# Kernel optimization log

Measured on AMD Instinct MI355X. Metric: run time of the kernel, lower is better.

The kernel has to match this reference:

```python
import jax, jax.numpy as jnp
import numpy as np

DIM = 512
HEADS = 8
DIM_HEAD = 64
HIDDEN = HEADS * DIM_HEAD  # 512
B, H, W = 32, 64, 64


def setup_inputs() -> dict:
    key = jax.random.key(0)
    k1, k2, k3 = jax.random.split(key, 3)
    x = jax.random.normal(k1, (B, H, W, DIM), dtype=jnp.float32)
    w_qkv = jax.random.normal(k2, (DIM, 3 * HIDDEN), dtype=jnp.float32) * 0.02
    w_out = jax.random.normal(k3, (HIDDEN, DIM), dtype=jnp.float32) * 0.02
    b_out = jnp.zeros((DIM,), dtype=jnp.float32)
    return {"x": x, "w_qkv": w_qkv, "w_out": w_out, "b_out": b_out}


def reference(x, w_qkv, w_out, b_out):
    b, h, w, c = x.shape
    n = h * w
    scale = DIM_HEAD ** (-0.5)
    # 1x1 conv (no bias) == matmul over channels
    qkv = jnp.einsum('bhwc,cf->bhwf', x, w_qkv)  # (b, h, w, 3*hidden)
    q, k, v = jnp.split(qkv, 3, axis=-1)
    # 'b x y (h c) -> b (x y) h c'
    def to_heads(t):
        return t.reshape(b, n, HEADS, DIM_HEAD)
    q, k, v = map(to_heads, (q, k, v))
    q = q * scale
    # contraction over spatial axis d=(x*y): sim (b, dim_head_i, heads, dim_head_j)
    sim = jnp.einsum('bdhi,bdhj->bihj', q, k)
    sim = sim - jnp.max(sim, axis=-1, keepdims=True)
    attn = jax.nn.softmax(sim, axis=-1)
    out = jnp.einsum('bihj,bdhj->bdhi', attn, v)  # (b, n, heads, dim_head)
    out = out.reshape(b, h, w, HIDDEN)
    # output 1x1 conv with bias
    return jnp.einsum('bhwf,fc->bhwc', out, w_out) + b_out
```

## Files before the change

kernel.cpp:

```cpp
#include <hip/hip_runtime.h>
#include <hip/hip_bf16.h>
#include <stdint.h>

using bf16x8 = __attribute__((ext_vector_type(8))) __bf16;
using s16x8  = __attribute__((ext_vector_type(8))) short;
using f32x4  = __attribute__((ext_vector_type(4))) float;

__device__ __forceinline__ uint16_t f2bf(float f) {
    uint32_t u = __builtin_bit_cast(uint32_t, f);
    u += 0x7fffu + ((u >> 16) & 1u);
    return (uint16_t)(u >> 16);
}
__device__ __forceinline__ float bf2f(uint16_t h) {
    return __builtin_bit_cast(float, (uint32_t)h << 16);
}

__device__ __forceinline__ void async16(uint16_t* lds_dst, const uint16_t* g_src) {
    __builtin_amdgcn_global_load_lds(
        (const __attribute__((address_space(1))) void*)g_src,
        (__attribute__((address_space(3))) void*)lds_dst,
        16, 0, 0);
}

__global__ __launch_bounds__(256, 4)
void xtw_k(const float* __restrict__ x, const float* __restrict__ wqkv,
           const float* __restrict__ wout,
           uint16_t* __restrict__ xb, uint16_t* __restrict__ xT,
           uint16_t* __restrict__ wqTs, uint16_t* __restrict__ wkTcat,
           uint16_t* __restrict__ woutT, uint16_t* __restrict__ wv_rm)
{
    __shared__ uint16_t lt[64 * 68];
    const int tid = threadIdx.x;
    const int bi = blockIdx.x;
    if (bi >= 16384) {
        int sec = (bi - 16384) >> 10;
        int idx = ((bi - 16384) & 1023) * 256 + tid;
        int co = idx >> 9, r = idx & 511;
        if (sec == 0) {
            wqTs[co * 512 + r] = f2bf(wqkv[r * 1536 + co] * 0.125f);
        } else if (sec == 1) {
            uint16_t v = f2bf(wqkv[r * 1536 + 512 + co]);
            wkTcat[co * 1024 + r] = v;
            wkTcat[co * 1024 + 512 + r] = v;
        } else if (sec == 2) {
            woutT[co * 512 + r] = f2bf(wout[r * 512 + co]);
        } else {
            wv_rm[co * 512 + r] = f2bf(wqkv[co * 1536 + 1024 + r]);
        }
        return;
    }
    const int b = bi >> 9;
    const int rem = bi & 511;
    const int st = rem >> 3, ct = rem & 7;
    const int c4 = (tid & 15) * 4;
#pragma unroll
    for (int rep = 0; rep < 4; ++rep) {
        int r = (tid >> 4) + rep * 16;
        long gs = (long)(b * 4096 + st * 64 + r) * 512 + ct * 64 + c4;
        float4 v = *(const float4*)(x + gs);
        uint16_t t[4];
        t[0] = f2bf(v.x); t[1] = f2bf(v.y); t[2] = f2bf(v.z); t[3] = f2bf(v.w);
        *(ushort4*)(xb + gs) = *(const ushort4*)t;
#pragma unroll
        for (int q = 0; q < 4; ++q) lt[r * 68 + c4 + q] = t[q];
    }
    __syncthreads();
    const int s4 = (tid & 15) * 4;
#pragma unroll
    for (int rep = 0; rep < 4; ++rep) {
        int c = (tid >> 4) + rep * 16;
        uint16_t t[4];
#pragma unroll
        for (int q = 0; q < 4; ++q) t[q] = lt[(s4 + q) * 68 + c];
        *(ushort4*)(xT + (long)(b * 512 + ct * 64 + c) * 4096 + st * 64 + s4) =
            *(const ushort4*)t;
    }
}

template<bool OUTF32>
__global__ __launch_bounds__(512, 2)
void g8_k(const uint16_t* __restrict__ A, const uint16_t* __restrict__ Bt,
          void* __restrict__ Cp, const float* __restrict__ bias,
          int K, int lda, int ldb, int ldc, int mtiles, int ntiles,
          long abr, long bbe, long cbr)
{
    __shared__ uint16_t lds[65536];
    const int tid  = threadIdx.x;
    const int lane = tid & 63;
    const int wv   = tid >> 6;
    const int wr   = wv >> 2, wc = wv & 3;

    const int q8 = gridDim.x >> 3;
    const int l  = (blockIdx.x & 7) * q8 + (blockIdx.x >> 3);
    const int per   = mtiles * ntiles;
    const int batch = l / per;
    const int rem   = l - batch * per;
    const int mt    = rem / ntiles, nt = rem - mt * ntiles;

    const long arow0 = abr * batch + (long)mt * 256;
    const uint16_t* abase = A + arow0 * (long)lda;
    const uint16_t* btb   = Bt + bbe * batch + (long)nt * 256 * ldb;

    const int fr = lane & 15;
    const int cx0 = (((0 << 2) | (lane >> 4)) ^ (fr & 7)) * 8;
    const int cx1 = (((1 << 2) | (lane >> 4)) ^ (fr & 7)) * 8;
    const int baseA = wr * 8192 + fr * 64;
    const int baseB = (2 + (wc >> 1)) * 8192 + ((wc & 1) * 64 + fr) * 64;

    const int NT = K >> 6;

    auto stage = [&](int slot, const uint16_t* gb, int rstride, int k0) {
#pragma unroll
        for (int i = 0; i < 2; ++i) {
            int si = i * 512 + wv * 64 + lane;
            int rr = si >> 3, cc = (si & 7) ^ (rr & 7);
            async16(&lds[slot * 8192 + (i * 512 + wv * 64) * 8],
                    gb + (long)rr * rstride + k0 + cc * 8);
        }
    };

    f32x4 acc[8][4];
#pragma unroll
    for (int m = 0; m < 8; ++m)
#pragma unroll
        for (int n = 0; n < 4; ++n) acc[m][n] = (f32x4){0.f, 0.f, 0.f, 0.f};

    bf16x8 af[4], bfq[4];

    auto rdA = [&](int mb, int b4, int cx) {
#pragma unroll
        for (int mi = 0; mi < 4; ++mi)
            af[mi] = __builtin_bit_cast(bf16x8,
                *(const s16x8*)&lds[b4 * 8192 + baseA + (mb + mi) * 1024 + cx]);
    };
    auto rdB = [&](int b4, int cx) {
#pragma unroll
        for (int n = 0; n < 4; ++n)
            bfq[n] = __builtin_bit_cast(bf16x8,
                *(const s16x8*)&lds[b4 * 8192 + baseB + n * 1024 + cx]);
    };
    auto mm = [&](int mb) {
        asm volatile("s_waitcnt lgkmcnt(0)" ::: "memory");
        __builtin_amdgcn_sched_barrier(0);
        __builtin_amdgcn_s_setprio(1);
#pragma unroll
        for (int mi = 0; mi < 4; ++mi)
#pragma unroll
            for (int n = 0; n < 4; ++n)
                acc[mb + mi][n] = __builtin_amdgcn_mfma_f32_16x16x32_bf16(
                    af[mi], bfq[n], acc[mb + mi][n], 0, 0, 0);
        __builtin_amdgcn_s_setprio(0);
        __builtin_amdgcn_s_barrier();
    };

    stage(0, abase,              lda, 0);
    stage(1, abase + 128L * lda, lda, 0);
    stage(2, btb,                ldb, 0);
    stage(3, btb + 128L * ldb,   ldb, 0);
    stage(6, btb,                ldb, 64);
    stage(7, btb + 128L * ldb,   ldb, 64);
    asm volatile("s_waitcnt vmcnt(4)" ::: "memory");
    __builtin_amdgcn_sched_barrier(0);
    __builtin_amdgcn_s_barrier();

    for (int it = 0; it < (NT >> 1); ++it) {
        const int E = 2 * it, Od = E + 1;
        const bool s3 = (E + 2) < NT;
        const bool s7 = (Od + 2) < NT;
        const int kE2 = (E + 2) << 6, kO1 = Od << 6, kO2 = (Od + 2) << 6;

        rdB(0, cx0); rdA(0, 0, cx0);
        stage(4, abase,              lda, kO1);
        stage(5, abase + 128L * lda, lda, kO1);
        __builtin_amdgcn_s_barrier();
        mm(0);
        rdA(4, 0, cx0);
        __builtin_amdgcn_s_barrier();
        mm(4);
        rdB(0, cx1); rdA(0, 0, cx1);
        __builtin_amdgcn_s_barrier();
        mm(0);
        rdA(4, 0, cx1);
        if (s3) {
            stage(2, btb,              ldb, kE2);
            stage(3, btb + 128L * ldb, ldb, kE2);
            asm volatile("s_waitcnt vmcnt(4)" ::: "memory");
        } else {
            asm volatile("s_waitcnt vmcnt(0)" ::: "memory");
        }
        __builtin_amdgcn_sched_barrier(0);
        __builtin_amdgcn_s_barrier();
        mm(4);
        rdB(4, cx0); rdA(0, 4, cx0);
        if (s3) {
            stage(0, abase,              lda, kE2);
            stage(1, abase + 128L * lda, lda, kE2);
        }
        __builtin_amdgcn_s_barrier();
        mm(0);
        rdA(4, 4, cx0);
        __builtin_amdgcn_s_barrier();
        mm(4);
        rdB(4, cx1); rdA(0, 4, cx1);
        __builtin_amdgcn_s_barrier();
        mm(0);
        rdA(4, 4, cx1);
        if (s7) {
            stage(6, btb,              ldb, kO2);
            stage(7, btb + 128L * ldb, ldb, kO2);
            asm volatile("s_waitcnt vmcnt(4)" ::: "memory");
        } else {
            asm volatile("s_waitcnt vmcnt(0)" ::: "memory");
        }
        __builtin_amdgcn_sched_barrier(0);
        __builtin_amdgcn_s_barrier();
        mm(4);
    }

    const long crow0 = cbr * batch + (long)mt * 256 + wr * 128;
    const int  col0  = nt * 256 + wc * 64;
    float bv[4];
#pragma unroll
    for (int n = 0; n < 4; ++n)
        bv[n] = bias ? bias[col0 + n * 16 + (lane & 15)] : 0.f;
#pragma unroll
    for (int m = 0; m < 8; ++m) {
#pragma unroll
        for (int r = 0; r < 4; ++r) {
            long row = crow0 + m * 16 + (lane >> 4) * 4 + r;
#pragma unroll
            for (int n = 0; n < 4; ++n) {
                int col = col0 + n * 16 + (lane & 15);
                float v = acc[m][n][r];
                if constexpr (OUTF32)
                    ((float*)Cp)[row * (long)ldc + col] = v + bv[n];
                else
                    ((uint16_t*)Cp)[row * (long)ldc + col] = f2bf(v);
            }
        }
    }
}

__global__ __launch_bounds__(512, 2)
void g8G_k(const uint16_t* __restrict__ X, uint16_t* __restrict__ Gcat)
{
    __shared__ uint16_t lds[65536];
    const int tid  = threadIdx.x;
    const int lane = tid & 63;
    const int wv   = tid >> 6;
    const int wr   = wv >> 2, wc = wv & 3;

    const int q8 = gridDim.x >> 3;
    const int l  = (blockIdx.x & 7) * q8 + (blockIdx.x >> 3);
    const int g  = l / 3;
    const int quad = l - g * 3;
    const int b = g >> 1, z = g & 1;
    const int mt = (quad == 1) ? 1 : 0;
    const int nt = (quad == 0) ? 0 : 1;

    const uint16_t* xb0 = X + (long)b * 512 * 4096 + z * 2048;
    const uint16_t* abase = xb0 + (long)mt * 256 * 4096;
    const uint16_t* btb   = xb0 + (long)nt * 256 * 4096;

    const int fr = lane & 15;
    const int cx0 = (((0 << 2) | (lane >> 4)) ^ (fr & 7)) * 8;
    const int cx1 = (((1 << 2) | (lane >> 4)) ^ (fr & 7)) * 8;
    const int baseA = wr * 8192 + fr * 64;
    const int baseB = (2 + (wc >> 1)) * 8192 + ((wc & 1) * 64 + fr) * 64;

    const int NT = 32;

    auto stage = [&](int slot, const uint16_t* gb, int k0) {
#pragma unroll
        for (int i = 0; i < 2; ++i) {
            int si = i * 512 + wv * 64 + lane;
            int rr = si >> 3, cc = (si & 7) ^ (rr & 7);
            async16(&lds[slot * 8192 + (i * 512 + wv * 64) * 8],
                    gb + (long)rr * 4096 + k0 + cc * 8);
        }
    };

    f32x4 acc[8][4];
#pragma unroll
    for (int m = 0; m < 8; ++m)
#pragma unroll
        for (int n = 0; n < 4; ++n) acc[m][n] = (f32x4){0.f, 0.f, 0.f, 0.f};

    bf16x8 af[4], bfq[4];
    auto rdA = [&](int mb, int b4, int cx) {
#pragma unroll
        for (int mi = 0; mi < 4; ++mi)
            af[mi] = __builtin_bit_cast(bf16x8,
                *(const s16x8*)&lds[b4 * 8192 + baseA + (mb + mi) * 1024 + cx]);
    };
    auto rdB = [&](int b4, int cx) {
#pragma unroll
        for (int n = 0; n < 4; ++n)
            bfq[n] = __builtin_bit_cast(bf16x8,
                *(const s16x8*)&lds[b4 * 8192 + baseB + n * 1024 + cx]);
    };
    auto mm = [&](int mb) {
        asm volatile("s_waitcnt lgkmcnt(0)" ::: "memory");
        __builtin_amdgcn_sched_barrier(0);
        __builtin_amdgcn_s_setprio(1);
#pragma unroll
        for (int mi = 0; mi < 4; ++mi)
#pragma unroll
            for (int n = 0; n < 4; ++n)
                acc[mb + mi][n] = __builtin_amdgcn_mfma_f32_16x16x32_bf16(
                    af[mi], bfq[n], acc[mb + mi][n], 0, 0, 0);
        __builtin_amdgcn_s_setprio(0);
        __builtin_amdgcn_s_barrier();
    };

    stage(0, abase,               0);
    stage(1, abase + 128L * 4096, 0);
    stage(2, btb,                 0);
    stage(3, btb + 128L * 4096,   0);
    stage(6, btb,                 64);
    stage(7, btb + 128L * 4096,   64);
    asm volatile("s_waitcnt vmcnt(4)" ::: "memory");
    __builtin_amdgcn_sched_barrier(0);
    __builtin_amdgcn_s_barrier();

    for (int it = 0; it < (NT >> 1); ++it) {
        const int E = 2 * it, Od = E + 1;
        const bool s3 = (E + 2) < NT;
        const bool s7 = (Od + 2) < NT;
        const int kE2 = (E + 2) << 6, kO1 = Od << 6, kO2 = (Od + 2) << 6;

        rdB(0, cx0); rdA(0, 0, cx0);
        stage(4, abase,               kO1);
        stage(5, abase + 128L * 4096, kO1);
        __builtin_amdgcn_s_barrier();
        mm(0);
        rdA(4, 0, cx0);
        __builtin_amdgcn_s_barrier();
        mm(4);
        rdB(0, cx1); rdA(0, 0, cx1);
        __builtin_amdgcn_s_barrier();
        mm(0);
        rdA(4, 0, cx1);
        if (s3) {
            stage(2, btb,               kE2);
            stage(3, btb + 128L * 4096, kE2);
            asm volatile("s_waitcnt vmcnt(4)" ::: "memory");
        } else {
            asm volatile("s_waitcnt vmcnt(0)" ::: "memory");
        }
        __builtin_amdgcn_sched_barrier(0);
        __builtin_amdgcn_s_barrier();
        mm(4);
        rdB(4, cx0); rdA(0, 4, cx0);
        if (s3) {
            stage(0, abase,               kE2);
            stage(1, abase + 128L * 4096, kE2);
        }
        __builtin_amdgcn_s_barrier();
        mm(0);
        rdA(4, 4, cx0);
        __builtin_amdgcn_s_barrier();
        mm(4);
        rdB(4, cx1); rdA(0, 4, cx1);
        __builtin_amdgcn_s_barrier();
        mm(0);
        rdA(4, 4, cx1);
        if (s7) {
            stage(6, btb,               kO2);
            stage(7, btb + 128L * 4096, kO2);
            asm volatile("s_waitcnt vmcnt(4)" ::: "memory");
        } else {
            asm volatile("s_waitcnt vmcnt(0)" ::: "memory");
        }
        __builtin_amdgcn_sched_barrier(0);
        __builtin_amdgcn_s_barrier();
        mm(4);
    }

    uint16_t* o = Gcat + (long)b * 524288;
    const int zoff = z * 512;
    const int row0 = mt * 256 + wr * 128;
    const int col0 = nt * 256 + wc * 64;
#pragma unroll
    for (int m = 0; m < 8; ++m) {
#pragma unroll
        for (int r = 0; r < 4; ++r) {
            int row = row0 + m * 16 + (lane >> 4) * 4 + r;
#pragma unroll
            for (int n = 0; n < 4; ++n)
                o[(long)row * 1024 + zoff + col0 + n * 16 + (lane & 15)] = f2bf(acc[m][n][r]);
        }
        if (quad == 2) {
            int rbase = row0 + m * 16 + (lane >> 4) * 4;
#pragma unroll
            for (int n = 0; n < 4; ++n) {
                int col = col0 + n * 16 + (lane & 15);
                uint16_t t[4];
#pragma unroll
                for (int r = 0; r < 4; ++r) t[r] = f2bf(acc[m][n][r]);
                *(ushort4*)&o[(long)col * 1024 + zoff + rbase] = *(const ushort4*)t;
            }
        }
    }
}

__global__ __launch_bounds__(512, 1)
void simfull_k(const uint16_t* __restrict__ Gcat, const uint16_t* __restrict__ wkTcat,
               const uint16_t* __restrict__ wqTs, uint16_t* __restrict__ attn)
{
    __shared__ uint16_t sm[73728];
    const int tid  = threadIdx.x;
    const int lane = tid & 63;
    const int wv   = tid >> 6;
    const int fr   = lane & 15;
    const int hi4  = lane >> 4;
    const int bi = blockIdx.x;
    const int h = bi >> 5;
    const int b = (bi & 7) * 4 + ((bi >> 3) & 3);

    const uint16_t* gb  = Gcat + (long)b * 524288;
    const uint16_t* ab  = wkTcat + (long)h * 64 * 1024;
    const uint16_t* qb2 = wqTs + (long)h * 64 * 512;

    auto stg = [&](int q, int t) {
        const int k0 = t * 32;
#pragma unroll
        for (int i = 0; i < 4; ++i) {
            int si = i * 64 + lane;
            int rr = si >> 2, cc = (si & 3) ^ ((rr >> 1) & 3);
            async16(&sm[q * 16384 + wv * 2048 + i * 512],
                    gb + (long)(wv * 64 + rr) * 1024 + k0 + cc * 8);
        }
        {
            int si = (wv & 3) * 64 + lane;
            int rr = si >> 2, cc = (si & 3) ^ ((rr >> 1) & 3);
            async16(&sm[49152 + q * 4096 + (wv >> 2) * 2048 + (wv & 3) * 512],
                    ab + (long)rr * 1024 + k0 + cc * 8);
        }
    };

    f32x4 acc[4][4];
#pragma unroll
    for (int mf = 0; mf < 4; ++mf)
#pragma unroll
        for (int nf = 0; nf < 4; ++nf) acc[mf][nf] = (f32x4){0.f, 0.f, 0.f, 0.f};

    const int sa = (hi4 ^ ((fr >> 1) & 3)) * 8;

    stg(0, 0);
    stg(1, 1);
    asm volatile("s_waitcnt vmcnt(5)" ::: "memory");
    __builtin_amdgcn_sched_barrier(0);
    __builtin_amdgcn_s_barrier();

    for (int t = 0; t < 32; ++t) {
        const int q = t % 3;
        if (t + 2 < 32) stg((t + 2) % 3, t + 2);
        bf16x8 af[4], bfq[4];
        const int wkb = 49152 + q * 4096 + (wv >> 2) * 2048;
#pragma unroll
        for (int mf = 0; mf < 4; ++mf)
            af[mf] = __builtin_bit_cast(bf16x8,
                *(const s16x8*)&sm[wkb + (mf * 16 + fr) * 32 + sa]);
#pragma unroll
        for (int nf = 0; nf < 4; ++nf)
            bfq[nf] = __builtin_bit_cast(bf16x8,
                *(const s16x8*)&sm[q * 16384 + wv * 2048 + (nf * 16 + fr) * 32 + sa]);
        asm volatile("s_waitcnt lgkmcnt(0)" ::: "memory");
        __builtin_amdgcn_sched_barrier(0);
        __builtin_amdgcn_s_setprio(1);
#pragma unroll
        for (int mf = 0; mf < 4; ++mf)
#pragma unroll
            for (int nf = 0; nf < 4; ++nf)
                acc[mf][nf] = __builtin_amdgcn_mfma_f32_16x16x32_bf16(
                    af[mf], bfq[nf], acc[mf][nf], 0, 0, 0);
        __builtin_amdgcn_s_setprio(0);
        if (t + 2 < 32) { asm volatile("s_waitcnt vmcnt(5)" ::: "memory"); }
        else            { asm volatile("s_waitcnt vmcnt(0)" ::: "memory"); }
        __builtin_amdgcn_sched_barrier(0);
        __builtin_amdgcn_s_barrier();
    }

#pragma unroll
    for (int mf = 0; mf < 4; ++mf)
#pragma unroll
        for (int nf = 0; nf < 4; ++nf)
#pragma unroll
            for (int r = 0; r < 4; ++r) {
                int j = mf * 16 + hi4 * 4 + r;
                int c = wv * 64 + nf * 16 + fr;
                float v = acc[mf][nf][r];
                uint16_t hi = f2bf(v);
                int off = j * 512 + ((c >> 3) ^ (j & 7)) * 8 + (c & 7);
                sm[off] = hi;
                sm[32768 + off] = f2bf(v - bf2f(hi));
            }
    __syncthreads();

    f32x4 a2[4][4];
#pragma unroll
    for (int mf = 0; mf < 4; ++mf)
#pragma unroll
        for (int nf = 0; nf < 4; ++nf) a2[mf][nf] = (f32x4){0.f, 0.f, 0.f, 0.f};
#pragma unroll
    for (int ks = 0; ks < 2; ++ks) {
        bf16x8 af[4], bh[4], bl[4];
#pragma unroll
        for (int mf = 0; mf < 4; ++mf)
            af[mf] = __builtin_bit_cast(bf16x8,
                *(const s16x8*)&qb2[(long)(mf * 16 + fr) * 512 + wv * 64 + ks * 32 + hi4 * 8]);
#pragma unroll
        for (int nf = 0; nf < 4; ++nf) {
            int j = nf * 16 + fr;
            int ch = (wv * 8 + ks * 4 + hi4) ^ (fr & 7);
            bh[nf] = __builtin_bit_cast(bf16x8, *(const s16x8*)&sm[j * 512 + ch * 8]);
            bl[nf] = __builtin_bit_cast(bf16x8, *(const s16x8*)&sm[32768 + j * 512 + ch * 8]);
        }
#pragma unroll
        for (int mf = 0; mf < 4; ++mf)
#pragma unroll
            for (int nf = 0; nf < 4; ++nf) {
                a2[mf][nf] = __builtin_amdgcn_mfma_f32_16x16x32_bf16(
                    af[mf], bh[nf], a2[mf][nf], 0, 0, 0);
                a2[mf][nf] = __builtin_amdgcn_mfma_f32_16x16x32_bf16(
                    af[mf], bl[nf], a2[mf][nf], 0, 0, 0);
            }
    }

    float* red = (float*)&sm[65536];
    for (int w = 0; w < 8; ++w) {
        if (wv == w) {
#pragma unroll
            for (int mf = 0; mf < 4; ++mf)
#pragma unroll
                for (int nf = 0; nf < 4; ++nf)
#pragma unroll
                    for (int r = 0; r < 4; ++r) {
                        int i = mf * 16 + hi4 * 4 + r;
                        int j = nf * 16 + fr;
                        float* p = &red[i * 64 + j];
                        *p = (w == 0) ? a2[mf][nf][r] : (*p + a2[mf][nf][r]);
                    }
        }
        __syncthreads();
    }

    float* rt1 = (float*)&sm[0];
    float* rt2 = (float*)&sm[512];
    const int i = tid >> 2, jc = tid & 3;
    float s[16];
    if (tid < 256) {
#pragma unroll
        for (int jj = 0; jj < 16; ++jj) s[jj] = red[i * 64 + jc * 16 + jj];
        float mx = s[0];
#pragma unroll
        for (int jj = 1; jj < 16; ++jj) mx = fmaxf(mx, s[jj]);
        rt1[i * 4 + jc] = mx;
    }
    __syncthreads();
    if (tid < 256) {
        float m4 = fmaxf(fmaxf(rt1[i * 4], rt1[i * 4 + 1]),
                         fmaxf(rt1[i * 4 + 2], rt1[i * 4 + 3]));
        float sum = 0.f;
#pragma unroll
        for (int jj = 0; jj < 16; ++jj) { s[jj] = __expf(s[jj] - m4); sum += s[jj]; }
        rt2[i * 4 + jc] = sum;
    }
    __syncthreads();
    if (tid < 256) {
        float tot = rt2[i * 4] + rt2[i * 4 + 1] + rt2[i * 4 + 2] + rt2[i * 4 + 3];
        float inv = 1.f / tot;
        uint16_t* at = attn + (long)(b * 8 + h) * 4096;
#pragma unroll
        for (int jj = 0; jj < 16; ++jj)
            at[i * 64 + jc * 16 + jj] = f2bf(s[jj] * inv);
    }
}

__global__ __launch_bounds__(512, 1)
void w2v_k(const uint16_t* __restrict__ attn, const uint16_t* __restrict__ woutT,
           const uint16_t* __restrict__ wv_rm, uint16_t* __restrict__ Bteff)
{
    __shared__ uint16_t RT[16384];
    const int tid  = threadIdx.x;
    const int lane = tid & 63;
    const int wv8  = tid >> 6;
    const int wr   = wv8 >> 2, wc = wv8 & 3;
    const int fr   = lane & 15;
    const int hi4  = lane >> 4;

    const int q8 = gridDim.x >> 3;
    const int l  = (blockIdx.x & 7) * q8 + (blockIdx.x >> 3);
    const int b  = l >> 2;
    const int mt = (l >> 1) & 1, nt = l & 1;

    f32x4 acc[8][4];
#pragma unroll
    for (int m = 0; m < 8; ++m)
#pragma unroll
        for (int n = 0; n < 4; ++n) acc[m][n] = (f32x4){0.f, 0.f, 0.f, 0.f};

    for (int h = 0; h < 8; ++h) {
        const uint16_t* ah = attn + (long)(b * 8 + h) * 4096;
        f32x4 rac[4][2];
#pragma unroll
        for (int mf = 0; mf < 4; ++mf)
#pragma unroll
            for (int nf = 0; nf < 2; ++nf) rac[mf][nf] = (f32x4){0.f, 0.f, 0.f, 0.f};
#pragma unroll
        for (int ks = 0; ks < 2; ++ks) {
            bf16x8 af[4], bf2[2];
#pragma unroll
            for (int mf = 0; mf < 4; ++mf)
                af[mf] = __builtin_bit_cast(bf16x8,
                    *(const s16x8*)&ah[(mf * 16 + fr) * 64 + ks * 32 + hi4 * 8]);
#pragma unroll
            for (int nf = 0; nf < 2; ++nf) {
                int k = nt * 256 + wv8 * 32 + nf * 16 + fr;
                bf2[nf] = __builtin_bit_cast(bf16x8,
                    *(const s16x8*)&wv_rm[(long)k * 512 + h * 64 + ks * 32 + hi4 * 8]);
            }
#pragma unroll
            for (int mf = 0; mf < 4; ++mf)
#pragma unroll
                for (int nf = 0; nf < 2; ++nf)
                    rac[mf][nf] = __builtin_amdgcn_mfma_f32_16x16x32_bf16(
                        af[mf], bf2[nf], rac[mf][nf], 0, 0, 0);
        }
        __syncthreads();
#pragma unroll
        for (int mf = 0; mf < 4; ++mf)
#pragma unroll
            for (int nf = 0; nf < 2; ++nf)
#pragma unroll
                for (int r = 0; r < 4; ++r) {
                    int i2 = mf * 16 + hi4 * 4 + r;
                    int k  = wv8 * 32 + nf * 16 + fr;
                    RT[k * 64 + (((i2 >> 3) ^ (k & 7)) * 8) + (i2 & 7)] = f2bf(rac[mf][nf][r]);
                }
        __syncthreads();
#pragma unroll
        for (int ks = 0; ks < 2; ++ks) {
            bf16x8 am[8], bm[4];
#pragma unroll
            for (int mf = 0; mf < 8; ++mf) {
                int c = mt * 256 + wr * 128 + mf * 16 + fr;
                am[mf] = __builtin_bit_cast(bf16x8,
                    *(const s16x8*)&woutT[(long)c * 512 + h * 64 + ks * 32 + hi4 * 8]);
            }
#pragma unroll
            for (int nf = 0; nf < 4; ++nf) {
                int k = wc * 64 + nf * 16 + fr;
                bm[nf] = __builtin_bit_cast(bf16x8,
                    *(const s16x8*)&RT[k * 64 + (((ks * 4 + hi4) ^ (k & 7)) * 8)]);
            }
#pragma unroll
            for (int mf = 0; mf < 8; ++mf)
#pragma unroll
                for (int nf = 0; nf < 4; ++nf)
                    acc[mf][nf] = __builtin_amdgcn_mfma_f32_16x16x32_bf16(
                        am[mf], bm[nf], acc[mf][nf], 0, 0, 0);
        }
    }

    uint16_t* o = Bteff + (long)b * 262144;
#pragma unroll
    for (int mf = 0; mf < 8; ++mf)
#pragma unroll
        for (int r = 0; r < 4; ++r) {
            int c = mt * 256 + wr * 128 + mf * 16 + hi4 * 4 + r;
#pragma unroll
            for (int nf = 0; nf < 4; ++nf) {
                int k = nt * 256 + wc * 64 + nf * 16 + fr;
                o[(long)c * 512 + k] = f2bf(acc[mf][nf][r]);
            }
        }
}

extern "C" void kernel_launch(void* const* d_in, const int* in_sizes, int n_in,
                              void* d_out, int out_size, void* d_ws, size_t ws_size,
                              hipStream_t stream)
{
    const float* x     = (const float*)d_in[0];
    const float* w_qkv = (const float*)d_in[1];
    const float* w_out = (const float*)d_in[2];
    const float* b_out = (const float*)d_in[3];
    float* out = (float*)d_out;

    char* ws = (char*)d_ws;
    uint16_t* xb     = (uint16_t*)(ws);
    uint16_t* xT     = (uint16_t*)(ws + 134217728L);
    uint16_t* Gcat   = (uint16_t*)(ws + 268435456L);
    uint16_t* attn   = (uint16_t*)(ws + 301989888L);
    uint16_t* Bteff  = (uint16_t*)(ws + 320864256L);
    uint16_t* wqTs   = (uint16_t*)(ws + 354418688L);
    uint16_t* wkTcat = (uint16_t*)(ws + 354942976L);
    uint16_t* woutT  = (uint16_t*)(ws + 355991552L);
    uint16_t* wv_rm  = (uint16_t*)(ws + 356515840L);

    xtw_k<<<20480, 256, 0, stream>>>(x, w_qkv, w_out, xb, xT,
                                     wqTs, wkTcat, woutT, wv_rm);

    g8G_k<<<192, 512, 0, stream>>>(xT, Gcat);

    simfull_k<<<256, 512, 0, stream>>>(Gcat, wkTcat, wqTs, attn);

    w2v_k<<<128, 512, 0, stream>>>(attn, woutT, wv_rm, Bteff);

    g8_k<true><<<1024, 512, 0, stream>>>(
        xb, Bteff, out, b_out,
        512, 512, 512, 512, 16, 2, 4096L, 262144L, 4096L);
}
```

Measured before the change: 393.0 us.

## Split Gram kernel into 128x128 triangular tiles with simpler single-buffer loop

```diff
diff --git a/kernel.cpp b/kernel.cpp
--- a/kernel.cpp
+++ b/kernel.cpp
@@ -241,148 +241,78 @@
     }
 }
 
-__global__ __launch_bounds__(512, 2)
-void g8G_k(const uint16_t* __restrict__ X, uint16_t* __restrict__ Gcat)
+__global__ __launch_bounds__(256, 4)
+void g128G_k(const uint16_t* __restrict__ X, uint16_t* __restrict__ Gcat)
 {
-    __shared__ uint16_t lds[65536];
+    __shared__ uint16_t Al[8192];
+    __shared__ uint16_t Bl[8192];
     const int tid  = threadIdx.x;
     const int lane = tid & 63;
     const int wv   = tid >> 6;
-    const int wr   = wv >> 2, wc = wv & 3;
+    const int wr   = wv >> 1, wc = wv & 1;
 
     const int q8 = gridDim.x >> 3;
     const int l  = (blockIdx.x & 7) * q8 + (blockIdx.x >> 3);
-    const int g  = l / 3;
-    const int quad = l - g * 3;
-    const int b = g >> 1, z = g & 1;
-    const int mt = (quad == 1) ? 1 : 0;
-    const int nt = (quad == 0) ? 0 : 1;
-
-    const uint16_t* xb0 = X + (long)b * 512 * 4096 + z * 2048;
-    const uint16_t* abase = xb0 + (long)mt * 256 * 4096;
-    const uint16_t* btb   = xb0 + (long)nt * 256 * 4096;
-
-    const int fr = lane & 15;
-    const int cx0 = (((0 << 2) | (lane >> 4)) ^ (fr & 7)) * 8;
-    const int cx1 = (((1 << 2) | (lane >> 4)) ^ (fr & 7)) * 8;
-    const int baseA = wr * 8192 + fr * 64;
-    const int baseB = (2 + (wc >> 1)) * 8192 + ((wc & 1) * 64 + fr) * 64;
-
-    const int NT = 32;
-
-    auto stage = [&](int slot, const uint16_t* gb, int k0) {
-#pragma unroll
-        for (int i = 0; i < 2; ++i) {
-            int si = i * 512 + wv * 64 + lane;
-            int rr = si >> 3, cc = (si & 7) ^ (rr & 7);
-            async16(&lds[slot * 8192 + (i * 512 + wv * 64) * 8],
-                    gb + (long)rr * 4096 + k0 + cc * 8);
-        }
-    };
-
-    f32x4 acc[8][4];
-#pragma unroll
-    for (int m = 0; m < 8; ++m)
+    const int g  = l / 10;
+    const int t  = l - g * 10;
+    const int i  = (t < 4) ? 0 : ((t < 7) ? 1 : ((t < 9) ? 2 : 3));
+    const int j  = t - ((i == 0) ? 0 : (i == 1) ? 3 : (i == 2) ? 5 : 6);
+    const int b  = g >> 1, z = g & 1;
+
+    const uint16_t* xz   = X + (long)b * 512 * 4096 + z * 2048;
+    const uint16_t* arow = xz + (long)i * 128 * 4096;
+    const uint16_t* brow = xz + (long)j * 128 * 4096;
+
+    f32x4 acc[4][4];
+#pragma unroll
+    for (int m = 0; m < 4; ++m)
 #pragma unroll
         for (int n = 0; n < 4; ++n) acc[m][n] = (f32x4){0.f, 0.f, 0.f, 0.f};
 
-    bf16x8 af[4], bfq[4];
-    auto rdA = [&](int mb, int b4, int cx) {
-#pragma unroll
-        for (int mi = 0; mi < 4; ++mi)
-            af[mi] = __builtin_bit_cast(bf16x8,
-                *(const s16x8*)&lds[b4 * 8192 + baseA + (mb + mi) * 1024 + cx]);
-    };
-    auto rdB = [&](int b4, int cx) {
-#pragma unroll
-        for (int n = 0; n < 4; ++n)
-            bfq[n] = __builtin_bit_cast(bf16x8,
-                *(const s16x8*)&lds[b4 * 8192 + baseB + n * 1024 + cx]);
-    };
-    auto mm = [&](int mb) {
-        asm volatile("s_waitcnt lgkmcnt(0)" ::: "memory");
-        __builtin_amdgcn_sched_barrier(0);
-        __builtin_amdgcn_s_setprio(1);
-#pragma unroll
-        for (int mi = 0; mi < 4; ++mi)
-#pragma unroll
-            for (int n = 0; n < 4; ++n)
-                acc[mb + mi][n] = __builtin_amdgcn_mfma_f32_16x16x32_bf16(
-                    af[mi], bfq[n], acc[mb + mi][n], 0, 0, 0);
-        __builtin_amdgcn_s_setprio(0);
-        __builtin_amdgcn_s_barrier();
-    };
-
-    stage(0, abase,               0);
-    stage(1, abase + 128L * 4096, 0);
-    stage(2, btb,                 0);
-    stage(3, btb + 128L * 4096,   0);
-    stage(6, btb,                 64);
-    stage(7, btb + 128L * 4096,   64);
-    asm volatile("s_waitcnt vmcnt(4)" ::: "memory");
-    __builtin_amdgcn_sched_barrier(0);
-    __builtin_amdgcn_s_barrier();
-
-    for (int it = 0; it < (NT >> 1); ++it) {
-        const int E = 2 * it, Od = E + 1;
-        const bool s3 = (E + 2) < NT;
-        const bool s7 = (Od + 2) < NT;
-        const int kE2 = (E + 2) << 6, kO1 = Od << 6, kO2 = (Od + 2) << 6;
-
-        rdB(0, cx0); rdA(0, 0, cx0);
-        stage(4, abase,               kO1);
-        stage(5, abase + 128L * 4096, kO1);
-        __builtin_amdgcn_s_barrier();
-        mm(0);
-        rdA(4, 0, cx0);
-        __builtin_amdgcn_s_barrier();
-        mm(4);
-        rdB(0, cx1); rdA(0, 0, cx1);
-        __builtin_amdgcn_s_barrier();
-        mm(0);
-        rdA(4, 0, cx1);
-        if (s3) {
-            stage(2, btb,               kE2);
-            stage(3, btb + 128L * 4096, kE2);
-            asm volatile("s_waitcnt vmcnt(4)" ::: "memory");
-        } else {
-            asm volatile("s_waitcnt vmcnt(0)" ::: "memory");
-        }
-        __builtin_amdgcn_sched_barrier(0);
-        __builtin_amdgcn_s_barrier();
-        mm(4);
-        rdB(4, cx0); rdA(0, 4, cx0);
-        if (s3) {
-            stage(0, abase,               kE2);
-            stage(1, abase + 128L * 4096, kE2);
-        }
-        __builtin_amdgcn_s_barrier();
-        mm(0);
-        rdA(4, 4, cx0);
-        __builtin_amdgcn_s_barrier();
-        mm(4);
-        rdB(4, cx1); rdA(0, 4, cx1);
-        __builtin_amdgcn_s_barrier();
-        mm(0);
-        rdA(4, 4, cx1);
-        if (s7) {
-            stage(6, btb,               kO2);
-            stage(7, btb + 128L * 4096, kO2);
-            asm volatile("s_waitcnt vmcnt(4)" ::: "memory");
-        } else {
-            asm volatile("s_waitcnt vmcnt(0)" ::: "memory");
-        }
-        __builtin_amdgcn_sched_barrier(0);
-        __builtin_amdgcn_s_barrier();
-        mm(4);
+    for (int k0 = 0; k0 < 2048; k0 += 64) {
+#pragma unroll
+        for (int s2 = 0; s2 < 4; ++s2) {
+            int cb  = s2 * 256 + wv * 64;
+            int ci  = cb + lane;
+            int row = ci >> 3;
+            int cs  = (ci & 7) ^ (row & 7);
+            async16(&Al[cb * 8], arow + (long)row * 4096 + k0 + cs * 8);
+            async16(&Bl[cb * 8], brow + (long)row * 4096 + k0 + cs * 8);
+        }
+        __syncthreads();
+#pragma unroll
+        for (int ks = 0; ks < 2; ++ks) {
+            bf16x8 af[4], bfr[4];
+#pragma unroll
+            for (int m = 0; m < 4; ++m) {
+                int row = wr * 64 + m * 16 + (lane & 15);
+                int ch  = ks * 4 + (lane >> 4);
+                s16x8 v = *(const s16x8*)&Al[row * 64 + ((ch ^ (row & 7)) * 8)];
+                af[m] = __builtin_bit_cast(bf16x8, v);
+            }
+#pragma unroll
+            for (int n = 0; n < 4; ++n) {
+                int row = wc * 64 + n * 16 + (lane & 15);
+                int ch  = ks * 4 + (lane >> 4);
+                s16x8 v = *(const s16x8*)&Bl[row * 64 + ((ch ^ (row & 7)) * 8)];
+                bfr[n] = __builtin_bit_cast(bf16x8, v);
+            }
+#pragma unroll
+            for (int m = 0; m < 4; ++m)
+#pragma unroll
+                for (int n = 0; n < 4; ++n)
+                    acc[m][n] = __builtin_amdgcn_mfma_f32_16x16x32_bf16(
+                        af[m], bfr[n], acc[m][n], 0, 0, 0);
+        }
+        __syncthreads();
     }
 
     uint16_t* o = Gcat + (long)b * 524288;
     const int zoff = z * 512;
-    const int row0 = mt * 256 + wr * 128;
-    const int col0 = nt * 256 + wc * 64;
-#pragma unroll
-    for (int m = 0; m < 8; ++m) {
+    const int row0 = i * 128 + wr * 64;
+    const int col0 = j * 128 + wc * 64;
+#pragma unroll
+    for (int m = 0; m < 4; ++m) {
 #pragma unroll
         for (int r = 0; r < 4; ++r) {
             int row = row0 + m * 16 + (lane >> 4) * 4 + r;
@@ -390,15 +320,15 @@
             for (int n = 0; n < 4; ++n)
                 o[(long)row * 1024 + zoff + col0 + n * 16 + (lane & 15)] = f2bf(acc[m][n][r]);
         }
-        if (quad == 2) {
+        if (i != j) {
             int rbase = row0 + m * 16 + (lane >> 4) * 4;
 #pragma unroll
             for (int n = 0; n < 4; ++n) {
                 int col = col0 + n * 16 + (lane & 15);
-                uint16_t t[4];
-#pragma unroll
-                for (int r = 0; r < 4; ++r) t[r] = f2bf(acc[m][n][r]);
-                *(ushort4*)&o[(long)col * 1024 + zoff + rbase] = *(const ushort4*)t;
+                uint16_t tt[4];
+#pragma unroll
+                for (int r = 0; r < 4; ++r) tt[r] = f2bf(acc[m][n][r]);
+                *(ushort4*)&o[(long)col * 1024 + zoff + rbase] = *(const ushort4*)tt;
             }
         }
     }
@@ -488,11 +418,11 @@
         for (int nf = 0; nf < 4; ++nf)
 #pragma unroll
             for (int r = 0; r < 4; ++r) {
-                int j = mf * 16 + hi4 * 4 + r;
+                int jj2 = mf * 16 + hi4 * 4 + r;
                 int c = wv * 64 + nf * 16 + fr;
                 float v = acc[mf][nf][r];
                 uint16_t hi = f2bf(v);
-                int off = j * 512 + ((c >> 3) ^ (j & 7)) * 8 + (c & 7);
+                int off = jj2 * 512 + ((c >> 3) ^ (jj2 & 7)) * 8 + (c & 7);
                 sm[off] = hi;
                 sm[32768 + off] = f2bf(v - bf2f(hi));
             }
@@ -512,10 +442,10 @@
                 *(const s16x8*)&qb2[(long)(mf * 16 + fr) * 512 + wv * 64 + ks * 32 + hi4 * 8]);
 #pragma unroll
         for (int nf = 0; nf < 4; ++nf) {
-            int j = nf * 16 + fr;
+            int jj2 = nf * 16 + fr;
             int ch = (wv * 8 + ks * 4 + hi4) ^ (fr & 7);
-            bh[nf] = __builtin_bit_cast(bf16x8, *(const s16x8*)&sm[j * 512 + ch * 8]);
-            bl[nf] = __builtin_bit_cast(bf16x8, *(const s16x8*)&sm[32768 + j * 512 + ch * 8]);
+            bh[nf] = __builtin_bit_cast(bf16x8, *(const s16x8*)&sm[jj2 * 512 + ch * 8]);
+            bl[nf] = __builtin_bit_cast(bf16x8, *(const s16x8*)&sm[32768 + jj2 * 512 + ch * 8]);
         }
 #pragma unroll
         for (int mf = 0; mf < 4; ++mf)
@@ -537,9 +467,9 @@
                 for (int nf = 0; nf < 4; ++nf)
 #pragma unroll
                     for (int r = 0; r < 4; ++r) {
-                        int i = mf * 16 + hi4 * 4 + r;
-                        int j = nf * 16 + fr;
-                        float* p = &red[i * 64 + j];
+                        int ii = mf * 16 + hi4 * 4 + r;
+                        int jj2 = nf * 16 + fr;
+                        float* p = &red[ii * 64 + jj2];
                         *p = (w == 0) ? a2[mf][nf][r] : (*p + a2[mf][nf][r]);
                     }
         }
@@ -548,33 +478,33 @@
 
     float* rt1 = (float*)&sm[0];
     float* rt2 = (float*)&sm[512];
-    const int i = tid >> 2, jc = tid & 3;
+    const int ii = tid >> 2, jc = tid & 3;
     float s[16];
     if (tid < 256) {
 #pragma unroll
-        for (int jj = 0; jj < 16; ++jj) s[jj] = red[i * 64 + jc * 16 + jj];
+        for (int jj = 0; jj < 16; ++jj) s[jj] = red[ii * 64 + jc * 16 + jj];
         float mx = s[0];
 #pragma unroll
         for (int jj = 1; jj < 16; ++jj) mx = fmaxf(mx, s[jj]);
-        rt1[i * 4 + jc] = mx;
+        rt1[ii * 4 + jc] = mx;
     }
     __syncthreads();
     if (tid < 256) {
-        float m4 = fmaxf(fmaxf(rt1[i * 4], rt1[i * 4 + 1]),
-                         fmaxf(rt1[i * 4 + 2], rt1[i * 4 + 3]));
+        float m4 = fmaxf(fmaxf(rt1[ii * 4], rt1[ii * 4 + 1]),
+                         fmaxf(rt1[ii * 4 + 2], rt1[ii * 4 + 3]));
         float sum = 0.f;
 #pragma unroll
         for (int jj = 0; jj < 16; ++jj) { s[jj] = __expf(s[jj] - m4); sum += s[jj]; }
-        rt2[i * 4 + jc] = sum;
+        rt2[ii * 4 + jc] = sum;
     }
     __syncthreads();
     if (tid < 256) {
-        float tot = rt2[i * 4] + rt2[i * 4 + 1] + rt2[i * 4 + 2] + rt2[i * 4 + 3];
+        float tot = rt2[ii * 4] + rt2[ii * 4 + 1] + rt2[ii * 4 + 2] + rt2[ii * 4 + 3];
         float inv = 1.f / tot;
         uint16_t* at = attn + (long)(b * 8 + h) * 4096;
 #pragma unroll
         for (int jj = 0; jj < 16; ++jj)
-            at[i * 64 + jc * 16 + jj] = f2bf(s[jj] * inv);
+            at[ii * 64 + jc * 16 + jj] = f2bf(s[jj] * inv);
     }
 }
 
@@ -702,7 +632,7 @@
     xtw_k<<<20480, 256, 0, stream>>>(x, w_qkv, w_out, xb, xT,
                                      wqTs, wkTcat, woutT, wv_rm);
 
-    g8G_k<<<192, 512, 0, stream>>>(xT, Gcat);
+    g128G_k<<<640, 256, 0, stream>>>(xT, Gcat);
 
     simfull_k<<<256, 512, 0, stream>>>(Gcat, wkTcat, wqTs, attn);
 
```

After: 391.8 us. Within noise of the previous version (-0.3%).
